# Performance work log

Hardware: AMD Instinct MI355X
Metric: run time of the kernel (lower is better)

The kernel has to match this reference:

```python
import jax, jax.numpy as jnp
import numpy as np

D_MODEL = 1024
H = 16
D_K = D_MODEL // H
EPS = 1e-8


def _feature_map(x):
    # elu(x) + 1 (Performer/linear-attention positive feature map)
    return jax.nn.elu(x) + 1.0


def setup_inputs() -> dict:
    key = jax.random.key(0)
    ks = jax.random.split(key, 8)
    B, L = 4, 2048
    q = jax.random.normal(ks[0], (B, L, D_MODEL), dtype=jnp.float32)
    k = jax.random.normal(ks[1], (B, L, D_MODEL), dtype=jnp.float32)
    v = jax.random.normal(ks[2], (B, L, D_MODEL), dtype=jnp.float32)
    mask = jnp.ones((B, 1, 1, L), dtype=bool)
    s = 1.0 / np.sqrt(D_MODEL)
    w_q = jax.random.normal(ks[3], (D_MODEL, D_MODEL), dtype=jnp.float32) * s
    w_k = jax.random.normal(ks[4], (D_MODEL, D_MODEL), dtype=jnp.float32) * s
    w_v = jax.random.normal(ks[5], (D_MODEL, D_MODEL), dtype=jnp.float32) * s
    w_o = jax.random.normal(ks[6], (D_MODEL, D_MODEL), dtype=jnp.float32) * s
    return {"q": q, "k": k, "v": v, "mask": mask,
            "w_q": w_q, "w_k": w_k, "w_v": w_v, "w_o": w_o}


def reference(q, k, v, mask, w_q, w_k, w_v, w_o):
    # Linear (use_Linear=True) branch of MultiHeadAttentionBlock.forward.
    B, Lq, _ = q.shape
    Lk = k.shape[1]
    # fused-style projections (torch Linear: x @ W.T), split into heads -> bhnd
    query = (q @ w_q.T).reshape(B, Lq, H, D_K).transpose(0, 2, 1, 3)
    key_  = (k @ w_k.T).reshape(B, Lk, H, D_K).transpose(0, 2, 1, 3)
    value = (v @ w_v.T).reshape(B, Lk, H, D_K).transpose(0, 2, 1, 3)

    Q = _feature_map(query)            # [B,H,Lq,d_k]
    K = _feature_map(key_)             # [B,H,Lk,d_k]
    KV = jnp.einsum('bhnd,bhnm->bhdm', K, value)           # [B,H,d_k,d_k]
    Z = 1.0 / (jnp.einsum('bhnd,bhd->bhn', Q, K.sum(axis=2)) + EPS)  # [B,H,Lq]
    out = jnp.einsum('bhnd,bhdm,bhn->bhnm', Q, KV, Z)      # [B,H,Lq,d_k]

    out = out.transpose(0, 2, 1, 3).reshape(B, Lq, D_MODEL)
    return out @ w_o.T
```

## Files before the change

kernel.cpp:

```cpp
#include <hip/hip_runtime.h>
#include <cstdint>
#include <cstddef>

typedef __bf16 bf16;
typedef __bf16 bf16x8 __attribute__((ext_vector_type(8)));
typedef __bf16 bf16x4 __attribute__((ext_vector_type(4)));
typedef float  f32x4  __attribute__((ext_vector_type(4)));

#define DM     1024
#define MROWS  8192
#define LSEQ   2048
#define NBATCH 4
#define NHEAD  16
#define BHEADS 64
#define KV_S   8
#define KVT_STRIDE 4160

__device__ __forceinline__ void async16(const void* g, void* l) {
    __builtin_amdgcn_global_load_lds(
        (const __attribute__((address_space(1))) void*)g,
        (__attribute__((address_space(3))) void*)l, 16, 0, 0);
}

struct CastArgs {
    const float* s[7];
    bf16*        d[7];
    int          nblk[7];
};

__global__ __launch_bounds__(256) void cast_all(CastArgs a) {
    const int z = blockIdx.z;
    if ((int)blockIdx.x >= a.nblk[z]) return;
    const int i = blockIdx.x * 256 + threadIdx.x;
    float4 f = ((const float4*)a.s[z])[i];
    bf16x4 o; o[0] = (bf16)f.x; o[1] = (bf16)f.y; o[2] = (bf16)f.z; o[3] = (bf16)f.w;
    ((bf16x4*)a.d[z])[i] = o;
}

struct GemmArgs {
    const bf16* A[3];
    const bf16* B[3];
    void*       C[3];
    int         mode[3];
    int         Ndim;
    int         Kdim;
};

__global__ __launch_bounds__(256) void gemm_nt(GemmArgs args) {
    const int z = blockIdx.z;
    const bf16* __restrict__ A  = args.A[z];
    const bf16* __restrict__ Bm = args.B[z];
    void* Cp = args.C[z];
    const int mode = args.mode[z];
    const int N = args.Ndim, K = args.Kdim;

    __shared__ __attribute__((aligned(16))) bf16 sA[128 * 64];
    __shared__ __attribute__((aligned(16))) bf16 sB[128 * 64];

    const int tid  = threadIdx.x;
    const int wave = tid >> 6;
    const int lane = tid & 63;
    const int wm = wave >> 1, wn = wave & 1;
    const int row0 = blockIdx.y * 128;
    const int col0 = blockIdx.x * 128;

    const int rr = lane >> 3;
    const int cc = lane & 7;
    const int csw = ((cc ^ rr) * 8);
    const bf16* gA = A  + (size_t)(row0 + wave * 32 + rr) * K + csw;
    const bf16* gB = Bm + (size_t)(col0 + wave * 32 + rr) * K + csw;

    f32x4 acc[4][4] = {};

    const int lr = lane & 15;
    const int qd = lane >> 4;
    const int swz = lr & 7;

    for (int k0 = 0; k0 < K; k0 += 64) {
        #pragma unroll
        for (int j = 0; j < 4; ++j) {
            async16(gA + k0 + (size_t)(j * 8) * K, &sA[(wave * 32 + j * 8) * 64]);
            async16(gB + k0 + (size_t)(j * 8) * K, &sB[(wave * 32 + j * 8) * 64]);
        }
        __syncthreads();

        #pragma unroll
        for (int ks = 0; ks < 2; ++ks) {
            bf16x8 af[4], bfr[4];
            #pragma unroll
            for (int mi = 0; mi < 4; ++mi)
                af[mi] = *(const bf16x8*)&sA[(wm * 64 + mi * 16 + lr) * 64 + (((ks * 4 + qd) ^ swz) * 8)];
            #pragma unroll
            for (int ni = 0; ni < 4; ++ni)
                bfr[ni] = *(const bf16x8*)&sB[(wn * 64 + ni * 16 + lr) * 64 + (((ks * 4 + qd) ^ swz) * 8)];
            #pragma unroll
            for (int mi = 0; mi < 4; ++mi)
                #pragma unroll
                for (int ni = 0; ni < 4; ++ni)
                    acc[mi][ni] = __builtin_amdgcn_mfma_f32_16x16x32_bf16(af[mi], bfr[ni], acc[mi][ni], 0, 0, 0);
        }
        __syncthreads();
    }

    #pragma unroll
    for (int mi = 0; mi < 4; ++mi) {
        #pragma unroll
        for (int ni = 0; ni < 4; ++ni) {
            #pragma unroll
            for (int r = 0; r < 4; ++r) {
                const int grow = row0 + wm * 64 + mi * 16 + qd * 4 + r;
                const int gcol = col0 + wn * 64 + ni * 16 + lr;
                float val = acc[mi][ni][r];
                if (mode == 1) val = (val > 0.f) ? (val + 1.f) : __expf(val);
                if (mode == 2) ((float*)Cp)[(size_t)grow * N + gcol] = val;
                else           ((bf16*)Cp)[(size_t)grow * N + gcol] = (bf16)val;
            }
        }
    }
}

__global__ __launch_bounds__(256) void kv_partial(const bf16* __restrict__ Kp,
                                                  const bf16* __restrict__ Vp,
                                                  float* __restrict__ KVTp) {
    const int bh = blockIdx.x, s = blockIdx.y;
    const int b = bh >> 4, h = bh & 15;
    const int tid = threadIdx.x;
    const int m  = tid & 63;
    const int dg = tid >> 6;

    __shared__ float sK[32][64];
    __shared__ float sV[32][64];

    float acc[16] = {};
    float ks = 0.f;

    const int rr = tid >> 3;
    const int cc = (tid & 7) * 8;

    const size_t rowbase = (size_t)(b * LSEQ + s * 256) * DM + h * 64;

    for (int c = 0; c < 8; ++c) {
        {
            const size_t g = rowbase + (size_t)(c * 32 + rr) * DM + cc;
            bf16x8 k8 = *(const bf16x8*)&Kp[g];
            bf16x8 v8 = *(const bf16x8*)&Vp[g];
            float4 kf0 = {(float)k8[0], (float)k8[1], (float)k8[2], (float)k8[3]};
            float4 kf1 = {(float)k8[4], (float)k8[5], (float)k8[6], (float)k8[7]};
            float4 vf0 = {(float)v8[0], (float)v8[1], (float)v8[2], (float)v8[3]};
            float4 vf1 = {(float)v8[4], (float)v8[5], (float)v8[6], (float)v8[7]};
            *(float4*)&sK[rr][cc]     = kf0;
            *(float4*)&sK[rr][cc + 4] = kf1;
            *(float4*)&sV[rr][cc]     = vf0;
            *(float4*)&sV[rr][cc + 4] = vf1;
        }
        __syncthreads();
        #pragma unroll 4
        for (int n = 0; n < 32; ++n) {
            const float vv = sV[n][m];
            const float4* pk = (const float4*)&sK[n][dg * 16];
            #pragma unroll
            for (int t4 = 0; t4 < 4; ++t4) {
                float4 kk = pk[t4];
                acc[t4 * 4 + 0] += vv * kk.x;
                acc[t4 * 4 + 1] += vv * kk.y;
                acc[t4 * 4 + 2] += vv * kk.z;
                acc[t4 * 4 + 3] += vv * kk.w;
            }
            if (dg == 0) ks += sK[n][m];
        }
        __syncthreads();
    }

    float* outp = &KVTp[(size_t)(bh * KV_S + s) * KVT_STRIDE];
    #pragma unroll
    for (int t4 = 0; t4 < 4; ++t4) {
        float4 o = {acc[t4 * 4 + 0], acc[t4 * 4 + 1], acc[t4 * 4 + 2], acc[t4 * 4 + 3]};
        *(float4*)&outp[m * 64 + dg * 16 + t4 * 4] = o;
    }
    if (dg == 0) outp[4096 + m] = ks;
}

__global__ __launch_bounds__(256) void kv_reduce(const float* __restrict__ KVTp,
                                                 bf16* __restrict__ KVT,
                                                 float* __restrict__ Ksum) {
    const int bh = blockIdx.x;
    const int idx = blockIdx.y * 256 + threadIdx.x;
    if (idx >= KVT_STRIDE) return;
    float s = 0.f;
    #pragma unroll
    for (int p = 0; p < KV_S; ++p) s += KVTp[(size_t)(bh * KV_S + p) * KVT_STRIDE + idx];
    if (idx < 4096) KVT[(size_t)bh * 4096 + idx] = (bf16)s;
    else            Ksum[bh * 64 + (idx - 4096)] = s;
}

__global__ __launch_bounds__(256) void z_kernel(const bf16* __restrict__ Qp,
                                                const float* __restrict__ Ksum,
                                                float* __restrict__ Z) {
    const int bh = blockIdx.x;
    const int b = bh >> 4, h = bh & 15;
    const int n = blockIdx.y * 256 + threadIdx.x;
    __shared__ float sks[64];
    if (threadIdx.x < 64) sks[threadIdx.x] = Ksum[bh * 64 + threadIdx.x];
    __syncthreads();
    const bf16* qrow = &Qp[(size_t)(b * LSEQ + n) * DM + h * 64];
    float acc = 0.f;
    #pragma unroll
    for (int c = 0; c < 8; ++c) {
        bf16x8 q8 = *(const bf16x8*)&qrow[c * 8];
        #pragma unroll
        for (int j = 0; j < 8; ++j) acc += (float)q8[j] * sks[c * 8 + j];
    }
    Z[(size_t)bh * LSEQ + n] = 1.0f / (acc + 1e-8f);
}

__global__ __launch_bounds__(256) void attn_out(const bf16* __restrict__ Qp,
                                                const bf16* __restrict__ KVT,
                                                const float* __restrict__ Z,
                                                bf16* __restrict__ Ab) {
    const int bh = blockIdx.y;
    const int b = bh >> 4, h = bh & 15;
    const int row0 = blockIdx.x * 128;
    const int tid = threadIdx.x, wave = tid >> 6, lane = tid & 63;

    __shared__ __attribute__((aligned(16))) bf16 sQ[128 * 64];
    __shared__ __attribute__((aligned(16))) bf16 sKV[64 * 64];

    const bf16* qbase = &Qp[(size_t)(b * LSEQ + row0) * DM + h * 64];
    #pragma unroll
    for (int j = 0; j < 4; ++j) {
        const int r0 = wave * 32 + j * 8;
        async16(qbase + (size_t)(r0 + (lane >> 3)) * DM + (lane & 7) * 8, &sQ[r0 * 64]);
    }
    const bf16* kvbase = &KVT[(size_t)bh * 4096];
    #pragma unroll
    for (int j = 0; j < 2; ++j) {
        const int r0 = wave * 16 + j * 8;
        async16(kvbase + (r0 + (lane >> 3)) * 64 + (lane & 7) * 8, &sKV[r0 * 64]);
    }
    __syncthreads();

    f32x4 acc[2][4] = {};
    const int lr = lane & 15, qd = lane >> 4;
    #pragma unroll
    for (int ks = 0; ks < 2; ++ks) {
        bf16x8 af[2], bfr[4];
        #pragma unroll
        for (int mi = 0; mi < 2; ++mi)
            af[mi] = *(const bf16x8*)&sQ[(wave * 32 + mi * 16 + lr) * 64 + ks * 32 + qd * 8];
        #pragma unroll
        for (int ni = 0; ni < 4; ++ni)
            bfr[ni] = *(const bf16x8*)&sKV[(ni * 16 + lr) * 64 + ks * 32 + qd * 8];
        #pragma unroll
        for (int mi = 0; mi < 2; ++mi)
            #pragma unroll
            for (int ni = 0; ni < 4; ++ni)
                acc[mi][ni] = __builtin_amdgcn_mfma_f32_16x16x32_bf16(af[mi], bfr[ni], acc[mi][ni], 0, 0, 0);
    }

    #pragma unroll
    for (int mi = 0; mi < 2; ++mi) {
        #pragma unroll
        for (int rr = 0; rr < 4; ++rr) {
            const int nrow = row0 + wave * 32 + mi * 16 + qd * 4 + rr;
            const float zv = Z[(size_t)bh * LSEQ + nrow];
            #pragma unroll
            for (int ni = 0; ni < 4; ++ni)
                Ab[(size_t)(b * LSEQ + nrow) * DM + h * 64 + ni * 16 + lr] =
                    (bf16)(acc[mi][ni][rr] * zv);
        }
    }
}

extern "C" void kernel_launch(void* const* d_in, const int* in_sizes, int n_in,
                              void* d_out, int out_size, void* d_ws, size_t ws_size,
                              hipStream_t stream) {
    const float* q  = (const float*)d_in[0];
    const float* k  = (const float*)d_in[1];
    const float* v  = (const float*)d_in[2];
    const float* wq = (const float*)d_in[4];
    const float* wk = (const float*)d_in[5];
    const float* wv = (const float*)d_in[6];
    const float* wo = (const float*)d_in[7];

    char* ws = (char*)d_ws;
    size_t off = 0;
    auto alloc = [&](size_t bytes) -> void* {
        void* p = ws + off;
        off += (bytes + 255) & ~(size_t)255;
        return p;
    };

    bf16* qb   = (bf16*)alloc((size_t)MROWS * DM * 2);
    bf16* kb   = (bf16*)alloc((size_t)MROWS * DM * 2);
    bf16* vb   = (bf16*)alloc((size_t)MROWS * DM * 2);
    bf16* wqb  = (bf16*)alloc((size_t)DM * DM * 2);
    bf16* wkb  = (bf16*)alloc((size_t)DM * DM * 2);
    bf16* wvb  = (bf16*)alloc((size_t)DM * DM * 2);
    bf16* wob  = (bf16*)alloc((size_t)DM * DM * 2);
    bf16* Qp   = (bf16*)alloc((size_t)MROWS * DM * 2);
    bf16* Kp   = (bf16*)alloc((size_t)MROWS * DM * 2);
    bf16* Vp   = (bf16*)alloc((size_t)MROWS * DM * 2);
    bf16* Ab   = (bf16*)alloc((size_t)MROWS * DM * 2);
    float* KVTp = (float*)alloc((size_t)BHEADS * KV_S * KVT_STRIDE * 4);
    bf16* KVT  = (bf16*)alloc((size_t)BHEADS * 4096 * 2);
    float* Ksum = (float*)alloc((size_t)BHEADS * 64 * 4);
    float* Z    = (float*)alloc((size_t)BHEADS * LSEQ * 4);

    CastArgs ca;
    ca.s[0] = q;  ca.s[1] = k;  ca.s[2] = v;  ca.s[3] = wq; ca.s[4] = wk; ca.s[5] = wv; ca.s[6] = wo;
    ca.d[0] = qb; ca.d[1] = kb; ca.d[2] = vb; ca.d[3] = wqb; ca.d[4] = wkb; ca.d[5] = wvb; ca.d[6] = wob;
    const int nb_big = MROWS * DM / 4 / 256, nb_w = DM * DM / 4 / 256;
    ca.nblk[0] = nb_big; ca.nblk[1] = nb_big; ca.nblk[2] = nb_big;
    ca.nblk[3] = nb_w; ca.nblk[4] = nb_w; ca.nblk[5] = nb_w; ca.nblk[6] = nb_w;
    cast_all<<<dim3(nb_big, 1, 7), 256, 0, stream>>>(ca);

    GemmArgs pa;
    pa.A[0] = qb;  pa.A[1] = kb;  pa.A[2] = vb;
    pa.B[0] = wqb; pa.B[1] = wkb; pa.B[2] = wvb;
    pa.C[0] = Qp;  pa.C[1] = Kp;  pa.C[2] = Vp;
    pa.mode[0] = 1; pa.mode[1] = 1; pa.mode[2] = 0;
    pa.Ndim = DM; pa.Kdim = DM;
    gemm_nt<<<dim3(DM / 128, MROWS / 128, 3), 256, 0, stream>>>(pa);

    kv_partial<<<dim3(BHEADS, KV_S), 256, 0, stream>>>(Kp, Vp, KVTp);
    kv_reduce<<<dim3(BHEADS, (KVT_STRIDE + 255) / 256), 256, 0, stream>>>(KVTp, KVT, Ksum);

    z_kernel<<<dim3(BHEADS, LSEQ / 256), 256, 0, stream>>>(Qp, Ksum, Z);

    attn_out<<<dim3(LSEQ / 128, BHEADS), 256, 0, stream>>>(Qp, KVT, Z, Ab);

    GemmArgs fa;
    fa.A[0] = Ab; fa.A[1] = nullptr; fa.A[2] = nullptr;
    fa.B[0] = wob; fa.B[1] = nullptr; fa.B[2] = nullptr;
    fa.C[0] = d_out; fa.C[1] = nullptr; fa.C[2] = nullptr;
    fa.mode[0] = 2; fa.mode[1] = 0; fa.mode[2] = 0;
    fa.Ndim = DM; fa.Kdim = DM;
    gemm_nt<<<dim3(DM / 128, MROWS / 128, 1), 256, 0, stream>>>(fa);
}
```

Baseline: 314.9 us.

## Fuse normalizer computation into attn_out, swizzle its LDS, and remap GEMM block order

```diff
diff --git a/kernel.cpp b/kernel.cpp
--- a/kernel.cpp
+++ b/kernel.cpp
@@ -61,8 +61,12 @@
     const int wave = tid >> 6;
     const int lane = tid & 63;
     const int wm = wave >> 1, wn = wave & 1;
-    const int row0 = blockIdx.y * 128;
-    const int col0 = blockIdx.x * 128;
+
+    const int fb = blockIdx.x + 8 * (int)blockIdx.y;
+    const int bx = (fb >> 3) & 7;
+    const int by = (fb & 7) * 8 + (fb >> 6);
+    const int row0 = by * 128;
+    const int col0 = bx * 128;
 
     const int rr = lane >> 3;
     const int cc = lane & 7;
@@ -193,29 +197,9 @@
     else            Ksum[bh * 64 + (idx - 4096)] = s;
 }
 
-__global__ __launch_bounds__(256) void z_kernel(const bf16* __restrict__ Qp,
-                                                const float* __restrict__ Ksum,
-                                                float* __restrict__ Z) {
-    const int bh = blockIdx.x;
-    const int b = bh >> 4, h = bh & 15;
-    const int n = blockIdx.y * 256 + threadIdx.x;
-    __shared__ float sks[64];
-    if (threadIdx.x < 64) sks[threadIdx.x] = Ksum[bh * 64 + threadIdx.x];
-    __syncthreads();
-    const bf16* qrow = &Qp[(size_t)(b * LSEQ + n) * DM + h * 64];
-    float acc = 0.f;
-    #pragma unroll
-    for (int c = 0; c < 8; ++c) {
-        bf16x8 q8 = *(const bf16x8*)&qrow[c * 8];
-        #pragma unroll
-        for (int j = 0; j < 8; ++j) acc += (float)q8[j] * sks[c * 8 + j];
-    }
-    Z[(size_t)bh * LSEQ + n] = 1.0f / (acc + 1e-8f);
-}
-
 __global__ __launch_bounds__(256) void attn_out(const bf16* __restrict__ Qp,
                                                 const bf16* __restrict__ KVT,
-                                                const float* __restrict__ Z,
+                                                const float* __restrict__ Ksum,
                                                 bf16* __restrict__ Ab) {
     const int bh = blockIdx.y;
     const int b = bh >> 4, h = bh & 15;
@@ -224,32 +208,56 @@
 
     __shared__ __attribute__((aligned(16))) bf16 sQ[128 * 64];
     __shared__ __attribute__((aligned(16))) bf16 sKV[64 * 64];
+    __shared__ float sKs[64];
+
+    const int rr8 = lane >> 3;
+    const int cc8 = lane & 7;
+    const int csw = ((cc8 ^ rr8) * 8);
 
     const bf16* qbase = &Qp[(size_t)(b * LSEQ + row0) * DM + h * 64];
     #pragma unroll
     for (int j = 0; j < 4; ++j) {
         const int r0 = wave * 32 + j * 8;
-        async16(qbase + (size_t)(r0 + (lane >> 3)) * DM + (lane & 7) * 8, &sQ[r0 * 64]);
+        async16(qbase + (size_t)(r0 + rr8) * DM + csw, &sQ[r0 * 64]);
     }
     const bf16* kvbase = &KVT[(size_t)bh * 4096];
     #pragma unroll
     for (int j = 0; j < 2; ++j) {
         const int r0 = wave * 16 + j * 8;
-        async16(kvbase + (r0 + (lane >> 3)) * 64 + (lane & 7) * 8, &sKV[r0 * 64]);
-    }
+        async16(kvbase + (r0 + rr8) * 64 + csw, &sKV[r0 * 64]);
+    }
+    if (tid < 64) sKs[tid] = Ksum[bh * 64 + tid];
     __syncthreads();
+
+    const int zrow = lane >> 1;
+    const int dh = lane & 1;
+    float zacc = 0.f;
+    {
+        const bf16* qr = &sQ[(wave * 32 + zrow) * 64];
+        #pragma unroll
+        for (int c = 0; c < 4; ++c) {
+            const int chunk = dh * 4 + c;
+            bf16x8 q8 = *(const bf16x8*)&qr[(chunk ^ (zrow & 7)) * 8];
+            const float* ksp = &sKs[chunk * 8];
+            #pragma unroll
+            for (int j = 0; j < 8; ++j) zacc += (float)q8[j] * ksp[j];
+        }
+    }
+    zacc += __shfl_xor(zacc, 1, 64);
+    const float zinv = 1.0f / (zacc + 1e-8f);
 
     f32x4 acc[2][4] = {};
     const int lr = lane & 15, qd = lane >> 4;
+    const int swz = lr & 7;
     #pragma unroll
     for (int ks = 0; ks < 2; ++ks) {
         bf16x8 af[2], bfr[4];
         #pragma unroll
         for (int mi = 0; mi < 2; ++mi)
-            af[mi] = *(const bf16x8*)&sQ[(wave * 32 + mi * 16 + lr) * 64 + ks * 32 + qd * 8];
+            af[mi] = *(const bf16x8*)&sQ[(wave * 32 + mi * 16 + lr) * 64 + (((ks * 4 + qd) ^ swz) * 8)];
         #pragma unroll
         for (int ni = 0; ni < 4; ++ni)
-            bfr[ni] = *(const bf16x8*)&sKV[(ni * 16 + lr) * 64 + ks * 32 + qd * 8];
+            bfr[ni] = *(const bf16x8*)&sKV[(ni * 16 + lr) * 64 + (((ks * 4 + qd) ^ swz) * 8)];
         #pragma unroll
         for (int mi = 0; mi < 2; ++mi)
             #pragma unroll
@@ -261,8 +269,9 @@
     for (int mi = 0; mi < 2; ++mi) {
         #pragma unroll
         for (int rr = 0; rr < 4; ++rr) {
-            const int nrow = row0 + wave * 32 + mi * 16 + qd * 4 + rr;
-            const float zv = Z[(size_t)bh * LSEQ + nrow];
+            const int rlocal = mi * 16 + qd * 4 + rr;
+            const float zv = __shfl(zinv, rlocal * 2, 64);
+            const int nrow = row0 + wave * 32 + rlocal;
             #pragma unroll
             for (int ni = 0; ni < 4; ++ni)
                 Ab[(size_t)(b * LSEQ + nrow) * DM + h * 64 + ni * 16 + lr] =
@@ -304,7 +313,6 @@
     float* KVTp = (float*)alloc((size_t)BHEADS * KV_S * KVT_STRIDE * 4);
     bf16* KVT  = (bf16*)alloc((size_t)BHEADS * 4096 * 2);
     float* Ksum = (float*)alloc((size_t)BHEADS * 64 * 4);
-    float* Z    = (float*)alloc((size_t)BHEADS * LSEQ * 4);
 
     CastArgs ca;
     ca.s[0] = q;  ca.s[1] = k;  ca.s[2] = v;  ca.s[3] = wq; ca.s[4] = wk; ca.s[5] = wv; ca.s[6] = wo;
@@ -325,9 +333,7 @@
     kv_partial<<<dim3(BHEADS, KV_S), 256, 0, stream>>>(Kp, Vp, KVTp);
     kv_reduce<<<dim3(BHEADS, (KVT_STRIDE + 255) / 256), 256, 0, stream>>>(KVTp, KVT, Ksum);
 
-    z_kernel<<<dim3(BHEADS, LSEQ / 256), 256, 0, stream>>>(Qp, Ksum, Z);
-
-    attn_out<<<dim3(LSEQ / 128, BHEADS), 256, 0, stream>>>(Qp, KVT, Z, Ab);
+    attn_out<<<dim3(LSEQ / 128, BHEADS), 256, 0, stream>>>(Qp, KVT, Ksum, Ab);
 
     GemmArgs fa;
     fa.A[0] = Ab; fa.A[1] = nullptr; fa.A[2] = nullptr;
```

Result: faster. 299.6 us (-4.8%).
